# Performance work log

Hardware: AMD Instinct MI355X
Metric: run time of the kernel (lower is better)

Reference implementation:

```python
import jax, jax.numpy as jnp
import numpy as np

B, N, D, LAT, EC = 1024, 256, 64, 128, 32


def setup_inputs() -> dict:
    key = jax.random.key(0)
    ks = jax.random.split(key, 8)
    s = lambda d: 1.0 / np.sqrt(d)
    return {
        "local_data": jax.random.normal(ks[0], (B, D), jnp.float32),
        "neighbor_data": jax.random.normal(ks[1], (B, N, D), jnp.float32),
        "Wc": jax.random.normal(ks[2], (D, EC), jnp.float32) * s(D),
        "bc": jnp.zeros((EC,), jnp.float32),
        "Wf": jax.random.normal(ks[3], (D, LAT), jnp.float32) * s(D),
        "bf": jnp.zeros((LAT,), jnp.float32),
        "Wa": jax.random.normal(ks[4], (3 * EC, LAT), jnp.float32) * s(3 * EC),
        "ba": jnp.zeros((LAT,), jnp.float32),
        "Wl": jax.random.normal(ks[5], (LAT, LAT), jnp.float32) * s(LAT),
        "bl": jnp.zeros((LAT,), jnp.float32),
    }


def reference(local_data, neighbor_data, Wc, bc, Wf, bf, Wa, ba, Wl, bl):
    # per-neighbor feature encoder: [B,N,LAT]
    enc_feature = jax.nn.relu(jnp.einsum("bnd,dk->bnk", neighbor_data, Wf) + bf)
    # per-neighbor communication encoder: [B,N,EC]
    enc_comm = jax.nn.relu(jnp.einsum("bnd,dk->bnk", neighbor_data, Wc) + bc)
    # self communication embedding: [B,EC]
    enc_comm_self = jax.nn.relu(local_data @ Wc + bc)
    # broadcast self and neighbor-mean to [B,N,EC]
    self_rep = jnp.broadcast_to(enc_comm_self[:, None, :], enc_comm.shape)
    mean_rep = jnp.broadcast_to(enc_comm.mean(axis=1, keepdims=True), enc_comm.shape)
    cat = jnp.concatenate([self_rep, enc_comm, mean_rep], axis=-1)  # [B,N,3*EC]
    # attention: linear then softmax over neighbor axis (dim=-2)
    att = jax.nn.softmax(jnp.einsum("bnc,ck->bnk", cat, Wa) + ba, axis=1)  # [B,N,LAT]
    # attention-weighted sum over neighbors: [B,LAT]
    aggregated = jnp.einsum("bnk,bnk->bk", att, enc_feature)
    # later layer
    return jax.nn.relu(aggregated @ Wl + bl)
```

## Files before the change

kernel.cpp:

```cpp
#include <hip/hip_runtime.h>

#define NB    256
#define DIN   64
#define LATD  128
#define ECD   32

typedef __attribute__((ext_vector_type(8))) __bf16 bf16x8;
typedef __attribute__((ext_vector_type(4))) float f32x4;

#define XS_STRIDE 72
#define EC_STRIDE 40
#define WA_STRIDE 40

#define WS_WC 0
#define WS_WF (32 * 72)
#define WS_WA (32 * 72 + 128 * 72)
#define WSTAGE_SHORTS (128 * 72 + 128 * 40)
#define WA_OFF (128 * 72)

#define MFMA(a, b, c) __builtin_amdgcn_mfma_f32_16x16x32_bf16((a), (b), (c), 0, 0, 0)

__device__ __forceinline__ unsigned short f2bf(float f) {
    unsigned u = __builtin_bit_cast(unsigned, f);
    u += 0x7fffu + ((u >> 16) & 1u);
    return (unsigned short)(u >> 16);
}

__device__ __forceinline__ unsigned cvt2(float lo, float hi) {
    unsigned r;
    asm("v_cvt_pk_bf16_f32 %0, %1, %2" : "=v"(r) : "v"(lo), "v"(hi));
    return r;
}

#if __has_builtin(__builtin_amdgcn_exp2f)
__device__ __forceinline__ float fexp2(float x) {
    return __builtin_amdgcn_exp2f(x);
}
#else
__device__ __forceinline__ float fexp2(float x) {
    float r;
    asm("v_exp_f32 %0, %1\n\ts_nop 1" : "=v"(r) : "v"(x));
    return r;
}
#endif

__device__ __forceinline__ bf16x8 pack8(float4 a, float4 b) {
    union { unsigned u[4]; bf16x8 v; } r;
    r.u[0] = cvt2(a.x, a.y);
    r.u[1] = cvt2(a.z, a.w);
    r.u[2] = cvt2(b.x, b.y);
    r.u[3] = cvt2(b.z, b.w);
    return r.v;
}

__device__ __forceinline__ void gload_lds16(const void* g, void* l) {
    __builtin_amdgcn_global_load_lds(
        (const __attribute__((address_space(1))) unsigned int*)g,
        (__attribute__((address_space(3))) unsigned int*)l, 16, 0, 0);
}

__global__ __launch_bounds__(256) void prep_kernel(
    const float* __restrict__ Wc, const float* __restrict__ Wf,
    const float* __restrict__ Wa, unsigned short* __restrict__ ws)
{
    int t = blockIdx.x * blockDim.x + threadIdx.x;
    int stride = gridDim.x * blockDim.x;
    for (int i = t; i < 32 * 64; i += stride) {
        int n = i >> 6, k = i & 63;
        ws[WS_WC + n * XS_STRIDE + k] = f2bf(Wc[k * ECD + n]);
    }
    for (int i = t; i < 128 * 64; i += stride) {
        int n = i >> 6, k = i & 63;
        ws[WS_WF + n * XS_STRIDE + k] = f2bf(Wf[k * LATD + n]);
    }
    for (int i = t; i < 128 * 32; i += stride) {
        int n = i >> 5, k = i & 31;
        ws[WS_WA + n * WA_STRIDE + k] = f2bf(Wa[(ECD + k) * LATD + n] * 1.44269504f);
    }
}

__global__ __launch_bounds__(256, 2) void arm_main(
    const float* __restrict__ xg,
    const float* __restrict__ bcv,
    const float* __restrict__ bfv,
    const float* __restrict__ wl,
    const float* __restrict__ blv,
    const unsigned short* __restrict__ ws,
    float* __restrict__ out)
{
    __shared__ unsigned short wstage[WSTAGE_SHORTS];
    __shared__ float bfs[LATD];
    __shared__ float xstage[4][1024];
    __shared__ unsigned short ecst[4][16 * EC_STRIDE];
    __shared__ float aggnum[2][4][LATD];
    __shared__ float aggden[2][4][LATD];
    __shared__ float aggfull[2][LATD];
    __shared__ float wlpart[2][2][LATD];

    const int b0   = blockIdx.x;
    const int b1   = blockIdx.x + 512;
    const int tid  = threadIdx.x;
    const int lane = tid & 63;
    const int w    = tid >> 6;
    const int l15  = lane & 15;
    const int q    = lane >> 4;

    uint4 wch[7];
    {
        const uint4* src = reinterpret_cast<const uint4*>(ws + WS_WF);
        #pragma unroll
        for (int i = 0; i < 7; ++i)
            wch[i] = src[tid + i * 256];
    }
    uint4 bfch;
    if (tid < 32) bfch = reinterpret_cast<const uint4*>(bfv)[tid];

    bf16x8 wfrag[2][2];
    #pragma unroll
    for (int ks = 0; ks < 2; ++ks)
        #pragma unroll
        for (int nb = 0; nb < 2; ++nb)
            wfrag[ks][nb] = *reinterpret_cast<const bf16x8*>(
                &ws[WS_WC + (nb * 16 + l15) * XS_STRIDE + ks * 32 + q * 8]);
    float bc0 = bcv[l15], bc1 = bcv[16 + l15];

    const float* xw0 = xg + (size_t)b0 * NB * DIN + w * 64 * DIN;
    const float* xw1 = xg + (size_t)b1 * NB * DIN + w * 64 * DIN;

#define STAGE(s_)                                                             \
    {                                                                         \
        const char* tb = (const char*)(((s_) < 4 ? xw0 : xw1) + ((s_) & 3) * 1024); \
        float* lb = &xstage[w][0];                                            \
        _Pragma("unroll")                                                     \
        for (int i = 0; i < 4; ++i) {                                         \
            unsigned off = (unsigned)(i * 1024 + lane * 16);                  \
            unsigned r7  = (unsigned)((i * 4 + q) & 7);                       \
            gload_lds16(tb + (off ^ (r7 << 4)), lb + i * 256);                \
        }                                                                     \
    }

    STAGE(0);

    {
        uint4* dst = reinterpret_cast<uint4*>(wstage);
        #pragma unroll
        for (int i = 0; i < 7; ++i)
            dst[tid + i * 256] = wch[i];
        if (tid < 32) reinterpret_cast<uint4*>(bfs)[tid] = bfch;
    }
    __syncthreads();

    float num[8] = {0.f, 0.f, 0.f, 0.f, 0.f, 0.f, 0.f, 0.f};
    float den[8] = {0.f, 0.f, 0.f, 0.f, 0.f, 0.f, 0.f, 0.f};

    const unsigned o0 = ((unsigned)(l15 * 256 + q * 32)) ^ ((unsigned)(l15 & 7) << 4);

    #pragma unroll 1
    for (int s = 0; s < 8; ++s) {
        asm volatile("s_waitcnt vmcnt(0)" ::: "memory");

        const char* xb = (const char*)&xstage[w][0];
        float4 r0 = *reinterpret_cast<const float4*>(xb + o0);
        float4 r1 = *reinterpret_cast<const float4*>(xb + (o0 ^ 16));
        float4 r2 = *reinterpret_cast<const float4*>(xb + (o0 ^ 128));
        float4 r3 = *reinterpret_cast<const float4*>(xb + (o0 ^ 144));

        asm volatile("s_waitcnt lgkmcnt(0)" ::: "memory");
        if (s < 7) { STAGE(s + 1); }

        bf16x8 xf0 = pack8(r0, r1);
        bf16x8 xf1 = pack8(r2, r3);

        f32x4 a0 = {bc0, bc0, bc0, bc0};
        f32x4 a1 = {bc1, bc1, bc1, bc1};
        a0 = MFMA(xf0, wfrag[0][0], a0); a0 = MFMA(xf1, wfrag[1][0], a0);
        a1 = MFMA(xf0, wfrag[0][1], a1); a1 = MFMA(xf1, wfrag[1][1], a1);
        #pragma unroll
        for (int r = 0; r < 4; ++r) {
            int row = q * 4 + r;
            unsigned pk = cvt2(fmaxf(a0[r], 0.f), fmaxf(a1[r], 0.f));
            ecst[w][row * EC_STRIDE + l15]      = (unsigned short)pk;
            ecst[w][row * EC_STRIDE + 16 + l15] = (unsigned short)(pk >> 16);
        }
        bf16x8 ecf = *reinterpret_cast<const bf16x8*>(&ecst[w][l15 * EC_STRIDE + q * 8]);

        #pragma unroll
        for (int g = 0; g < 8; ++g) {
            const int rw = g * 16 + l15;
            bf16x8 wf0 = *reinterpret_cast<const bf16x8*>(&wstage[rw * XS_STRIDE + q * 8]);
            bf16x8 wf1 = *reinterpret_cast<const bf16x8*>(&wstage[rw * XS_STRIDE + 32 + q * 8]);
            bf16x8 wag = *reinterpret_cast<const bf16x8*>(&wstage[WA_OFF + rw * WA_STRIDE + q * 8]);
            float  bfl = bfs[rw];

            f32x4 z = {bfl, bfl, bfl, bfl};
            z = MFMA(xf0, wf0, z);
            f32x4 ef = MFMA(xf1, wf1, z);
            f32x4 zz = {0.f, 0.f, 0.f, 0.f};
            f32x4 lg = MFMA(ecf, wag, zz);
            #pragma unroll
            for (int r = 0; r < 4; ++r) {
                float ev = fmaxf(ef[r], 0.f);
                float p  = fexp2(lg[r]);
                num[g] = fmaf(p, ev, num[g]);
                den[g] += p;
            }
        }

        if ((s & 3) == 3) {
            const int e = s >> 2;
            #pragma unroll
            for (int g = 0; g < 8; ++g) {
                float n2 = num[g], d2 = den[g];
                n2 += __shfl_xor(n2, 16, 64); n2 += __shfl_xor(n2, 32, 64);
                d2 += __shfl_xor(d2, 16, 64); d2 += __shfl_xor(d2, 32, 64);
                if (lane < 16) {
                    aggnum[e][w][g * 16 + lane] = n2;
                    aggden[e][w][g * 16 + lane] = d2;
                }
                num[g] = 0.f;
                den[g] = 0.f;
            }
        }
    }
#undef STAGE
    __syncthreads();

    {
        int e = tid >> 7, c = tid & 127;
        float n2 = aggnum[e][0][c] + aggnum[e][1][c] + aggnum[e][2][c] + aggnum[e][3][c];
        float d2 = aggden[e][0][c] + aggden[e][1][c] + aggden[e][2][c] + aggden[e][3][c];
        aggfull[e][c] = n2 / d2;
    }
    __syncthreads();

    {
        int c = tid & 127, h = tid >> 7;
        float acc0 = 0.f, acc1 = 0.f;
        #pragma unroll 16
        for (int k = h * 64; k < h * 64 + 64; ++k) {
            float wv = wl[k * LATD + c];
            acc0 = fmaf(aggfull[0][k], wv, acc0);
            acc1 = fmaf(aggfull[1][k], wv, acc1);
        }
        wlpart[h][0][c] = acc0;
        wlpart[h][1][c] = acc1;
    }
    __syncthreads();
    {
        int e = tid >> 7, c = tid & 127;
        out[(size_t)(e ? b1 : b0) * LATD + c] =
            fmaxf(wlpart[0][e][c] + wlpart[1][e][c] + blv[c], 0.f);
    }
}

extern "C" void kernel_launch(void* const* d_in, const int* in_sizes, int n_in,
                              void* d_out, int out_size, void* d_ws, size_t ws_size,
                              hipStream_t stream)
{
    const float* xg  = (const float*)d_in[1];
    const float* wc  = (const float*)d_in[2];
    const float* bc_ = (const float*)d_in[3];
    const float* wf  = (const float*)d_in[4];
    const float* bf_ = (const float*)d_in[5];
    const float* wa  = (const float*)d_in[6];
    const float* wl  = (const float*)d_in[8];
    const float* bl_ = (const float*)d_in[9];
    unsigned short* wsp = (unsigned short*)d_ws;
    float* out = (float*)d_out;

    prep_kernel<<<8, 256, 0, stream>>>(wc, wf, wa, wsp);
    arm_main<<<512, 256, 0, stream>>>(xg, bc_, bf_, wl, bl_, wsp, out);
}
```

Baseline: 121.9 us.

## Use one batch per block and read weights from global instead of LDS

The kernel now runs 1024 blocks, each handling one batch element, instead of 512 blocks handling two each. It drops the LDS staging of Wf, Wa and bf and loads those weight fragments straight from global memory (relying on the cache), software-prefetching the next group's fragments inside the inner loop. Launch bounds rise to 4 blocks per CU so more waves can hide latency. The cost is repeated global/L2 weight loads per stage and more register pressure from the prefetch, in exchange for less LDS use and no staging barrier.

```diff
diff --git a/kernel.cpp b/kernel.cpp
--- a/kernel.cpp
+++ b/kernel.cpp
@@ -15,8 +15,6 @@
 #define WS_WC 0
 #define WS_WF (32 * 72)
 #define WS_WA (32 * 72 + 128 * 72)
-#define WSTAGE_SHORTS (128 * 72 + 128 * 40)
-#define WA_OFF (128 * 72)
 
 #define MFMA(a, b, c) __builtin_amdgcn_mfma_f32_16x16x32_bf16((a), (b), (c), 0, 0, 0)
 
@@ -79,7 +77,7 @@
     }
 }
 
-__global__ __launch_bounds__(256, 2) void arm_main(
+__global__ __launch_bounds__(256, 4) void arm_main(
     const float* __restrict__ xg,
     const float* __restrict__ bcv,
     const float* __restrict__ bfv,
@@ -88,32 +86,19 @@
     const unsigned short* __restrict__ ws,
     float* __restrict__ out)
 {
-    __shared__ unsigned short wstage[WSTAGE_SHORTS];
-    __shared__ float bfs[LATD];
     __shared__ float xstage[4][1024];
     __shared__ unsigned short ecst[4][16 * EC_STRIDE];
-    __shared__ float aggnum[2][4][LATD];
-    __shared__ float aggden[2][4][LATD];
-    __shared__ float aggfull[2][LATD];
-    __shared__ float wlpart[2][2][LATD];
-
-    const int b0   = blockIdx.x;
-    const int b1   = blockIdx.x + 512;
+    __shared__ float aggnum[4][LATD];
+    __shared__ float aggden[4][LATD];
+    __shared__ float aggfull[LATD];
+    __shared__ float wlpart[2][LATD];
+
+    const int b    = blockIdx.x;
     const int tid  = threadIdx.x;
     const int lane = tid & 63;
     const int w    = tid >> 6;
     const int l15  = lane & 15;
     const int q    = lane >> 4;
-
-    uint4 wch[7];
-    {
-        const uint4* src = reinterpret_cast<const uint4*>(ws + WS_WF);
-        #pragma unroll
-        for (int i = 0; i < 7; ++i)
-            wch[i] = src[tid + i * 256];
-    }
-    uint4 bfch;
-    if (tid < 32) bfch = reinterpret_cast<const uint4*>(bfv)[tid];
 
     bf16x8 wfrag[2][2];
     #pragma unroll
@@ -124,12 +109,11 @@
                 &ws[WS_WC + (nb * 16 + l15) * XS_STRIDE + ks * 32 + q * 8]);
     float bc0 = bcv[l15], bc1 = bcv[16 + l15];
 
-    const float* xw0 = xg + (size_t)b0 * NB * DIN + w * 64 * DIN;
-    const float* xw1 = xg + (size_t)b1 * NB * DIN + w * 64 * DIN;
+    const float* xw = xg + (size_t)b * NB * DIN + w * 64 * DIN;
 
 #define STAGE(s_)                                                             \
     {                                                                         \
-        const char* tb = (const char*)(((s_) < 4 ? xw0 : xw1) + ((s_) & 3) * 1024); \
+        const char* tb = (const char*)(xw + (s_) * 1024);                     \
         float* lb = &xstage[w][0];                                            \
         _Pragma("unroll")                                                     \
         for (int i = 0; i < 4; ++i) {                                         \
@@ -141,22 +125,16 @@
 
     STAGE(0);
 
-    {
-        uint4* dst = reinterpret_cast<uint4*>(wstage);
-        #pragma unroll
-        for (int i = 0; i < 7; ++i)
-            dst[tid + i * 256] = wch[i];
-        if (tid < 32) reinterpret_cast<uint4*>(bfs)[tid] = bfch;
-    }
-    __syncthreads();
-
     float num[8] = {0.f, 0.f, 0.f, 0.f, 0.f, 0.f, 0.f, 0.f};
     float den[8] = {0.f, 0.f, 0.f, 0.f, 0.f, 0.f, 0.f, 0.f};
 
     const unsigned o0 = ((unsigned)(l15 * 256 + q * 32)) ^ ((unsigned)(l15 & 7) << 4);
 
+    const unsigned short* wfb = ws + WS_WF;
+    const unsigned short* wab = ws + WS_WA;
+
     #pragma unroll 1
-    for (int s = 0; s < 8; ++s) {
+    for (int s = 0; s < 4; ++s) {
         asm volatile("s_waitcnt vmcnt(0)" ::: "memory");
 
         const char* xb = (const char*)&xstage[w][0];
@@ -166,7 +144,7 @@
         float4 r3 = *reinterpret_cast<const float4*>(xb + (o0 ^ 144));
 
         asm volatile("s_waitcnt lgkmcnt(0)" ::: "memory");
-        if (s < 7) { STAGE(s + 1); }
+        if (s < 3) { STAGE(s + 1); }
 
         bf16x8 xf0 = pack8(r0, r1);
         bf16x8 xf1 = pack8(r2, r3);
@@ -184,13 +162,22 @@
         }
         bf16x8 ecf = *reinterpret_cast<const bf16x8*>(&ecst[w][l15 * EC_STRIDE + q * 8]);
 
+        bf16x8 wf0 = *reinterpret_cast<const bf16x8*>(&wfb[l15 * XS_STRIDE + q * 8]);
+        bf16x8 wf1 = *reinterpret_cast<const bf16x8*>(&wfb[l15 * XS_STRIDE + 32 + q * 8]);
+        bf16x8 wag = *reinterpret_cast<const bf16x8*>(&wab[l15 * WA_STRIDE + q * 8]);
+        float  bfl = bfv[l15];
+
         #pragma unroll
         for (int g = 0; g < 8; ++g) {
-            const int rw = g * 16 + l15;
-            bf16x8 wf0 = *reinterpret_cast<const bf16x8*>(&wstage[rw * XS_STRIDE + q * 8]);
-            bf16x8 wf1 = *reinterpret_cast<const bf16x8*>(&wstage[rw * XS_STRIDE + 32 + q * 8]);
-            bf16x8 wag = *reinterpret_cast<const bf16x8*>(&wstage[WA_OFF + rw * WA_STRIDE + q * 8]);
-            float  bfl = bfs[rw];
+            bf16x8 nwf0, nwf1, nwag;
+            float  nbfl = 0.f;
+            if (g < 7) {
+                int rn = (g + 1) * 16 + l15;
+                nwf0 = *reinterpret_cast<const bf16x8*>(&wfb[rn * XS_STRIDE + q * 8]);
+                nwf1 = *reinterpret_cast<const bf16x8*>(&wfb[rn * XS_STRIDE + 32 + q * 8]);
+                nwag = *reinterpret_cast<const bf16x8*>(&wab[rn * WA_STRIDE + q * 8]);
+                nbfl = bfv[rn];
+            }
 
             f32x4 z = {bfl, bfl, bfl, bfl};
             z = MFMA(xf0, wf0, z);
@@ -204,53 +191,43 @@
                 num[g] = fmaf(p, ev, num[g]);
                 den[g] += p;
             }
+
+            if (g < 7) { wf0 = nwf0; wf1 = nwf1; wag = nwag; bfl = nbfl; }
         }
-
-        if ((s & 3) == 3) {
-            const int e = s >> 2;
-            #pragma unroll
-            for (int g = 0; g < 8; ++g) {
-                float n2 = num[g], d2 = den[g];
-                n2 += __shfl_xor(n2, 16, 64); n2 += __shfl_xor(n2, 32, 64);
-                d2 += __shfl_xor(d2, 16, 64); d2 += __shfl_xor(d2, 32, 64);
-                if (lane < 16) {
-                    aggnum[e][w][g * 16 + lane] = n2;
-                    aggden[e][w][g * 16 + lane] = d2;
-                }
-                num[g] = 0.f;
-                den[g] = 0.f;
-            }
+    }
+#undef STAGE
+
+    #pragma unroll
+    for (int g = 0; g < 8; ++g) {
+        float n2 = num[g], d2 = den[g];
+        n2 += __shfl_xor(n2, 16, 64); n2 += __shfl_xor(n2, 32, 64);
+        d2 += __shfl_xor(d2, 16, 64); d2 += __shfl_xor(d2, 32, 64);
+        if (lane < 16) {
+            aggnum[w][g * 16 + lane] = n2;
+            aggden[w][g * 16 + lane] = d2;
         }
     }
-#undef STAGE
     __syncthreads();
 
-    {
-        int e = tid >> 7, c = tid & 127;
-        float n2 = aggnum[e][0][c] + aggnum[e][1][c] + aggnum[e][2][c] + aggnum[e][3][c];
-        float d2 = aggden[e][0][c] + aggden[e][1][c] + aggden[e][2][c] + aggden[e][3][c];
-        aggfull[e][c] = n2 / d2;
+    if (tid < 128) {
+        float n2 = aggnum[0][tid] + aggnum[1][tid] + aggnum[2][tid] + aggnum[3][tid];
+        float d2 = aggden[0][tid] + aggden[1][tid] + aggden[2][tid] + aggden[3][tid];
+        aggfull[tid] = n2 / d2;
     }
     __syncthreads();
 
     {
         int c = tid & 127, h = tid >> 7;
-        float acc0 = 0.f, acc1 = 0.f;
+        float acc = 0.f;
         #pragma unroll 16
-        for (int k = h * 64; k < h * 64 + 64; ++k) {
-            float wv = wl[k * LATD + c];
-            acc0 = fmaf(aggfull[0][k], wv, acc0);
-            acc1 = fmaf(aggfull[1][k], wv, acc1);
-        }
-        wlpart[h][0][c] = acc0;
-        wlpart[h][1][c] = acc1;
+        for (int k = h * 64; k < h * 64 + 64; ++k)
+            acc = fmaf(aggfull[k], wl[k * LATD + c], acc);
+        wlpart[h][c] = acc;
     }
     __syncthreads();
-    {
-        int e = tid >> 7, c = tid & 127;
-        out[(size_t)(e ? b1 : b0) * LATD + c] =
-            fmaxf(wlpart[0][e][c] + wlpart[1][e][c] + blv[c], 0.f);
-    }
+    if (tid < 128)
+        out[(size_t)b * LATD + tid] =
+            fmaxf(wlpart[0][tid] + wlpart[1][tid] + blv[tid], 0.f);
 }
 
 extern "C" void kernel_launch(void* const* d_in, const int* in_sizes, int n_in,
@@ -269,5 +246,5 @@
     float* out = (float*)d_out;
 
     prep_kernel<<<8, 256, 0, stream>>>(wc, wf, wa, wsp);
-    arm_main<<<512, 256, 0, stream>>>(xg, bc_, bf_, wl, bl_, wsp, out);
-}
+    arm_main<<<1024, 256, 0, stream>>>(xg, bc_, bf_, wl, bl_, wsp, out);
+}
```

Result: slower. 168.1 us (+37.9%).
